# Optimization experiments

Measured on AMD Instinct MI355X. Metric: run time of the kernel, lower is better.

## Reference

```python
import jax, jax.numpy as jnp
import numpy as np

B, T, H, Q = 64, 2048, 512, 512


def setup_inputs() -> dict:
    key = jax.random.key(0)
    k1, k2, k3, k4, k5 = jax.random.split(key, 5)
    query = jax.random.normal(k1, (B, Q), dtype=jnp.float32)
    encoder_outputs = jax.random.normal(k2, (B, T, H), dtype=jnp.float32)
    # nn.Linear(hidden_size, query_size): weight [Q, H], bias [Q]
    W = jax.random.normal(k3, (Q, H), dtype=jnp.float32) * (1.0 / np.sqrt(H))
    b = jax.random.normal(k4, (Q,), dtype=jnp.float32) * 0.01
    tgt_index = jax.random.randint(k5, (B,), 0, T, dtype=jnp.int64)
    return {"query": query, "encoder_outputs": encoder_outputs, "W": W, "b": b,
            "tgt_index": tgt_index}


def reference(query, encoder_outputs, W, b, tgt_index):
    # method == 'general': energy[b,i] = (W @ enc[b,i] + bias) . query[b]
    proj = jnp.einsum('bth,qh->btq', encoder_outputs, W) + b       # [B,T,Q]
    energies = jnp.einsum('btq,bq->bt', proj, query)               # [B,T]
    # ragged mask: position i valid iff i <= tgt_index[b] (this_len = tgt_index+1)
    mask = jnp.arange(T)[None, :] <= tgt_index[:, None]            # [B,T]
    logits = jnp.where(mask, energies, -jnp.inf)
    attn = jax.nn.softmax(logits, axis=-1)                         # [B,T]
    context = jnp.einsum('bt,bth->bh', attn, encoder_outputs)      # [B,H]
    return context
```

## Files before the change

kernel.cpp:

```cpp
#include <hip/hip_runtime.h>
#include <hip/hip_bf16.h>
#include <math.h>


#define B 64
#define T 2048
#define H 512
#define Q 512
#define TT 128
#define NCH (T / TT)

__global__ void k_proj(const float* __restrict__ query,
                       const float* __restrict__ W,
                       const float* __restrict__ bias,
                       float* __restrict__ v,
                       float* __restrict__ c) {
    int b = blockIdx.y;
    int tid = threadIdx.x;
    int h = blockIdx.x * 128 + tid;

    __shared__ float sq[Q];
    for (int i = tid; i < Q; i += 128) sq[i] = query[(size_t)b * Q + i];
    __syncthreads();

    float acc = 0.0f;
#pragma unroll 8
    for (int q = 0; q < Q; ++q) acc += sq[q] * W[(size_t)q * H + h];
    v[(size_t)b * H + h] = acc;

    if (blockIdx.x == 0) {
        float pb = 0.0f;
        for (int i = tid; i < Q; i += 128) pb += sq[i] * bias[i];
        for (int off = 32; off; off >>= 1) pb += __shfl_xor(pb, off, 64);
        __shared__ float sred[2];
        if ((tid & 63) == 0) sred[tid >> 6] = pb;
        __syncthreads();
        if (tid == 0) c[b] = sred[0] + sred[1];
    }
}

__global__ __launch_bounds__(256) void k_attn(const float* __restrict__ enc,
                                              const float* __restrict__ v,
                                              const float* __restrict__ c,
                                              const int* __restrict__ tgt,
                                              float* __restrict__ pm,
                                              float* __restrict__ pl,
                                              float* __restrict__ pctx) {
    int b = blockIdx.y;
    int len = tgt[b] + 1;
    int t0 = blockIdx.x * TT;
    if (t0 >= len) return;
    int n = min(TT, len - t0);

    int tid = threadIdx.x;
    int wave = tid >> 6;
    int lane = tid & 63;

    const float4* v4 = (const float4*)(v + (size_t)b * H);
    float4 w0 = v4[lane];
    float4 w1 = v4[lane + 64];
    float cb = c[b];

    float m = -INFINITY, l = 0.0f;
    float4 a0 = {0.f,0.f,0.f,0.f}, a1 = {0.f,0.f,0.f,0.f};
    const float* encb = enc + ((size_t)b * T + t0) * H;

    for (int t = wave * 4; t < n; t += 16) {
        const float4* r0 = (const float4*)(encb + (size_t)(t + 0) * H);
        const float4* r1 = (const float4*)(encb + (size_t)(t + 1) * H);
        const float4* r2 = (const float4*)(encb + (size_t)(t + 2) * H);
        const float4* r3 = (const float4*)(encb + (size_t)(t + 3) * H);
        float4 x00 = r0[lane], x01 = r0[lane + 64];
        float4 x10 = r1[lane], x11 = r1[lane + 64];
        float4 x20 = r2[lane], x21 = r2[lane + 64];
        float4 x30 = r3[lane], x31 = r3[lane + 64];

        float e0 = x00.x*w0.x + x00.y*w0.y + x00.z*w0.z + x00.w*w0.w
                 + x01.x*w1.x + x01.y*w1.y + x01.z*w1.z + x01.w*w1.w;
        float e1 = x10.x*w0.x + x10.y*w0.y + x10.z*w0.z + x10.w*w0.w
                 + x11.x*w1.x + x11.y*w1.y + x11.z*w1.z + x11.w*w1.w;
        float e2 = x20.x*w0.x + x20.y*w0.y + x20.z*w0.z + x20.w*w0.w
                 + x21.x*w1.x + x21.y*w1.y + x21.z*w1.z + x21.w*w1.w;
        float e3 = x30.x*w0.x + x30.y*w0.y + x30.z*w0.z + x30.w*w0.w
                 + x31.x*w1.x + x31.y*w1.y + x31.z*w1.z + x31.w*w1.w;

        for (int off = 32; off; off >>= 1) {
            e0 += __shfl_xor(e0, off, 64);
            e1 += __shfl_xor(e1, off, 64);
            e2 += __shfl_xor(e2, off, 64);
            e3 += __shfl_xor(e3, off, 64);
        }
        e0 += cb;
        e1 = (t + 1 < n) ? e1 + cb : -INFINITY;
        e2 = (t + 2 < n) ? e2 + cb : -INFINITY;
        e3 = (t + 3 < n) ? e3 + cb : -INFINITY;

        float mn = fmaxf(fmaxf(fmaxf(e0, e1), fmaxf(e2, e3)), m);
        float alpha = __expf(m - mn);
        float p0 = __expf(e0 - mn);
        float p1 = __expf(e1 - mn);
        float p2 = __expf(e2 - mn);
        float p3 = __expf(e3 - mn);
        l = l * alpha + (p0 + p1) + (p2 + p3);
        a0.x = a0.x*alpha + p0*x00.x + p1*x10.x + p2*x20.x + p3*x30.x;
        a0.y = a0.y*alpha + p0*x00.y + p1*x10.y + p2*x20.y + p3*x30.y;
        a0.z = a0.z*alpha + p0*x00.z + p1*x10.z + p2*x20.z + p3*x30.z;
        a0.w = a0.w*alpha + p0*x00.w + p1*x10.w + p2*x20.w + p3*x30.w;
        a1.x = a1.x*alpha + p0*x01.x + p1*x11.x + p2*x21.x + p3*x31.x;
        a1.y = a1.y*alpha + p0*x01.y + p1*x11.y + p2*x21.y + p3*x31.y;
        a1.z = a1.z*alpha + p0*x01.z + p1*x11.z + p2*x21.z + p3*x31.z;
        a1.w = a1.w*alpha + p0*x01.w + p1*x11.w + p2*x21.w + p3*x31.w;
        m = mn;
    }

    __shared__ float sm4[4], sl4[4];
    __shared__ float sctx[4 * H];
    float4* sc = (float4*)(sctx + wave * H);
    sc[lane]      = a0;
    sc[lane + 64] = a1;
    if (lane == 0) { sm4[wave] = m; sl4[wave] = l; }
    __syncthreads();

    float M = fmaxf(fmaxf(sm4[0], sm4[1]), fmaxf(sm4[2], sm4[3]));
    float L = 0.0f, acc0 = 0.0f, acc1 = 0.0f;
#pragma unroll
    for (int j = 0; j < 4; ++j) {
        float mj = sm4[j];
        float wj = (mj == -INFINITY) ? 0.0f : __expf(mj - M);
        L += sl4[j] * wj;
        acc0 += wj * sctx[j * H + 2 * tid];
        acc1 += wj * sctx[j * H + 2 * tid + 1];
    }
    int pidx = b * NCH + blockIdx.x;
    if (tid == 0) { pm[pidx] = M; pl[pidx] = L; }
    float2* dst = (float2*)(pctx + (size_t)pidx * H);
    dst[tid] = make_float2(acc0, acc1);
}

__global__ void k_combine(const float* __restrict__ pm,
                          const float* __restrict__ pl,
                          const float* __restrict__ pctx,
                          const int* __restrict__ tgt,
                          float* __restrict__ out) {
    int b = blockIdx.x;
    int tid = threadIdx.x;
    int len = tgt[b] + 1;
    int nch = (len + TT - 1) / TT;

    __shared__ float spm[NCH], spl[NCH];
    if (tid < nch) {
        spm[tid] = pm[b * NCH + tid];
        spl[tid] = pl[b * NCH + tid];
    }
    __syncthreads();

    float M = -INFINITY;
    for (int j = 0; j < nch; ++j) M = fmaxf(M, spm[j]);
    float L = 0.0f;
    for (int j = 0; j < nch; ++j) L += spl[j] * __expf(spm[j] - M);
    float invL = 1.0f / L;

    float acc0 = 0.0f, acc1 = 0.0f;
    for (int j = 0; j < nch; ++j) {
        float wj = __expf(spm[j] - M) * invL;
        float2 x = ((const float2*)(pctx + (size_t)(b * NCH + j) * H))[tid];
        acc0 += wj * x.x;
        acc1 += wj * x.y;
    }
    out[(size_t)b * H + 2 * tid]     = acc0;
    out[(size_t)b * H + 2 * tid + 1] = acc1;
}

extern "C" void kernel_launch(void* const* d_in, const int* in_sizes, int n_in,
                              void* d_out, int out_size, void* d_ws, size_t ws_size,
                              hipStream_t stream) {
    const float* query = (const float*)d_in[0];
    const float* enc   = (const float*)d_in[1];
    const float* W     = (const float*)d_in[2];
    const float* bias  = (const float*)d_in[3];
    const int*   tgt   = (const int*)d_in[4];
    float* out = (float*)d_out;

    char* ws = (char*)d_ws;
    float* v    = (float*)ws;  ws += (size_t)B * H * sizeof(float);
    float* c    = (float*)ws;  ws += 256;
    float* pm   = (float*)ws;  ws += (size_t)B * NCH * sizeof(float);
    float* pl   = (float*)ws;  ws += (size_t)B * NCH * sizeof(float);
    float* pctx = (float*)ws;

    k_proj<<<dim3(H / 128, B), dim3(128), 0, stream>>>(query, W, bias, v, c);
    k_attn<<<dim3(NCH, B), dim3(256), 0, stream>>>(enc, v, c, tgt, pm, pl, pctx);
    k_combine<<<dim3(B), dim3(256), 0, stream>>>(pm, pl, pctx, tgt, out);
}
```

Measured before the change: 378.5 us.

## Fuse combine into attention via last-block atomic counter and vectorize projection kernel

```diff
diff --git a/kernel.cpp b/kernel.cpp
--- a/kernel.cpp
+++ b/kernel.cpp
@@ -1,5 +1,4 @@
 #include <hip/hip_runtime.h>
-#include <hip/hip_bf16.h>
 #include <math.h>
 
 
@@ -10,32 +9,56 @@
 #define TT 128
 #define NCH (T / TT)
 
-__global__ void k_proj(const float* __restrict__ query,
-                       const float* __restrict__ W,
-                       const float* __restrict__ bias,
-                       float* __restrict__ v,
-                       float* __restrict__ c) {
+__global__ __launch_bounds__(256) void k_proj(const float* __restrict__ query,
+                                              const float* __restrict__ W,
+                                              const float* __restrict__ bias,
+                                              float* __restrict__ v,
+                                              float* __restrict__ c,
+                                              int* __restrict__ cnt) {
     int b = blockIdx.y;
     int tid = threadIdx.x;
-    int h = blockIdx.x * 128 + tid;
+    int lane = tid & 63;
+    int qq = tid >> 6;
+    int h4 = blockIdx.x * 256 + lane * 4;
 
     __shared__ float sq[Q];
-    for (int i = tid; i < Q; i += 128) sq[i] = query[(size_t)b * Q + i];
-    __syncthreads();
-
-    float acc = 0.0f;
+    ((float2*)sq)[tid] = ((const float2*)(query + (size_t)b * Q))[tid];
+    __syncthreads();
+
+    float4 acc = {0.f, 0.f, 0.f, 0.f};
+    const float* Wp = W + (size_t)(qq * 128) * H + h4;
 #pragma unroll 8
-    for (int q = 0; q < Q; ++q) acc += sq[q] * W[(size_t)q * H + h];
-    v[(size_t)b * H + h] = acc;
+    for (int q = 0; q < 128; ++q) {
+        float s = sq[qq * 128 + q];
+        const float4 w = *(const float4*)(Wp + (size_t)q * H);
+        acc.x += s * w.x; acc.y += s * w.y;
+        acc.z += s * w.z; acc.w += s * w.w;
+    }
+
+    __shared__ float4 sp[4][64];
+    sp[qq][lane] = acc;
+    __syncthreads();
+    if (qq == 0) {
+        float4 r0 = sp[0][lane], r1 = sp[1][lane];
+        float4 r2 = sp[2][lane], r3 = sp[3][lane];
+        float4 r;
+        r.x = (r0.x + r1.x) + (r2.x + r3.x);
+        r.y = (r0.y + r1.y) + (r2.y + r3.y);
+        r.z = (r0.z + r1.z) + (r2.z + r3.z);
+        r.w = (r0.w + r1.w) + (r2.w + r3.w);
+        ((float4*)(v + (size_t)b * H))[blockIdx.x * 64 + lane] = r;
+    }
 
     if (blockIdx.x == 0) {
-        float pb = 0.0f;
-        for (int i = tid; i < Q; i += 128) pb += sq[i] * bias[i];
+        float pb = sq[tid] * bias[tid] + sq[tid + 256] * bias[tid + 256];
         for (int off = 32; off; off >>= 1) pb += __shfl_xor(pb, off, 64);
-        __shared__ float sred[2];
-        if ((tid & 63) == 0) sred[tid >> 6] = pb;
+        __shared__ float sred[4];
+        if (lane == 0) sred[qq] = pb;
         __syncthreads();
-        if (tid == 0) c[b] = sred[0] + sred[1];
+        if (tid == 0) {
+            c[b] = (sred[0] + sred[1]) + (sred[2] + sred[3]);
+            cnt[b] = 0;
+        }
     }
 }
 
@@ -45,12 +68,15 @@
                                               const int* __restrict__ tgt,
                                               float* __restrict__ pm,
                                               float* __restrict__ pl,
-                                              float* __restrict__ pctx) {
+                                              float* __restrict__ pctx,
+                                              int* __restrict__ cnt,
+                                              float* __restrict__ out) {
     int b = blockIdx.y;
     int len = tgt[b] + 1;
     int t0 = blockIdx.x * TT;
     if (t0 >= len) return;
     int n = min(TT, len - t0);
+    int nch = (len + TT - 1) / TT;
 
     int tid = threadIdx.x;
     int wave = tid >> 6;
@@ -135,17 +161,16 @@
     if (tid == 0) { pm[pidx] = M; pl[pidx] = L; }
     float2* dst = (float2*)(pctx + (size_t)pidx * H);
     dst[tid] = make_float2(acc0, acc1);
-}
-
-__global__ void k_combine(const float* __restrict__ pm,
-                          const float* __restrict__ pl,
-                          const float* __restrict__ pctx,
-                          const int* __restrict__ tgt,
-                          float* __restrict__ out) {
-    int b = blockIdx.x;
-    int tid = threadIdx.x;
-    int len = tgt[b] + 1;
-    int nch = (len + TT - 1) / TT;
+
+    __syncthreads();
+    __shared__ int slast;
+    if (tid == 0) {
+        __threadfence();
+        slast = (atomicAdd(&cnt[b], 1) == nch - 1);
+    }
+    __syncthreads();
+    if (!slast) return;
+    __threadfence();
 
     __shared__ float spm[NCH], spl[NCH];
     if (tid < nch) {
@@ -154,21 +179,21 @@
     }
     __syncthreads();
 
-    float M = -INFINITY;
-    for (int j = 0; j < nch; ++j) M = fmaxf(M, spm[j]);
-    float L = 0.0f;
-    for (int j = 0; j < nch; ++j) L += spl[j] * __expf(spm[j] - M);
-    float invL = 1.0f / L;
-
-    float acc0 = 0.0f, acc1 = 0.0f;
+    float M2 = -INFINITY;
+    for (int j = 0; j < nch; ++j) M2 = fmaxf(M2, spm[j]);
+    float L2 = 0.0f;
+    for (int j = 0; j < nch; ++j) L2 += spl[j] * __expf(spm[j] - M2);
+    float invL = 1.0f / L2;
+
+    float o0 = 0.0f, o1 = 0.0f;
     for (int j = 0; j < nch; ++j) {
-        float wj = __expf(spm[j] - M) * invL;
+        float wj = __expf(spm[j] - M2) * invL;
         float2 x = ((const float2*)(pctx + (size_t)(b * NCH + j) * H))[tid];
-        acc0 += wj * x.x;
-        acc1 += wj * x.y;
-    }
-    out[(size_t)b * H + 2 * tid]     = acc0;
-    out[(size_t)b * H + 2 * tid + 1] = acc1;
+        o0 += wj * x.x;
+        o1 += wj * x.y;
+    }
+    out[(size_t)b * H + 2 * tid]     = o0;
+    out[(size_t)b * H + 2 * tid + 1] = o1;
 }
 
 extern "C" void kernel_launch(void* const* d_in, const int* in_sizes, int n_in,
@@ -186,9 +211,10 @@
     float* c    = (float*)ws;  ws += 256;
     float* pm   = (float*)ws;  ws += (size_t)B * NCH * sizeof(float);
     float* pl   = (float*)ws;  ws += (size_t)B * NCH * sizeof(float);
-    float* pctx = (float*)ws;
-
-    k_proj<<<dim3(H / 128, B), dim3(128), 0, stream>>>(query, W, bias, v, c);
-    k_attn<<<dim3(NCH, B), dim3(256), 0, stream>>>(enc, v, c, tgt, pm, pl, pctx);
-    k_combine<<<dim3(B), dim3(256), 0, stream>>>(pm, pl, pctx, tgt, out);
+    float* pctx = (float*)ws;  ws += (size_t)B * NCH * H * sizeof(float);
+    int*   cnt  = (int*)ws;
+
+    k_proj<<<dim3(2, B), dim3(256), 0, stream>>>(query, W, bias, v, c, cnt);
+    k_attn<<<dim3(NCH, B), dim3(256), 0, stream>>>(enc, v, c, tgt,
+                                                   pm, pl, pctx, cnt, out);
 }
```

Result: slower. 470.1 us (+24.2%).

## Shrink attention chunk size and vectorize projection kernel with split-Q reduction

Applied to the files above, without the earlier changes.

```diff
diff --git a/kernel.cpp b/kernel.cpp
--- a/kernel.cpp
+++ b/kernel.cpp
@@ -1,5 +1,4 @@
 #include <hip/hip_runtime.h>
-#include <hip/hip_bf16.h>
 #include <math.h>
 
 
@@ -7,35 +6,55 @@
 #define T 2048
 #define H 512
 #define Q 512
-#define TT 128
+#define TT 32
 #define NCH (T / TT)
 
-__global__ void k_proj(const float* __restrict__ query,
-                       const float* __restrict__ W,
-                       const float* __restrict__ bias,
-                       float* __restrict__ v,
-                       float* __restrict__ c) {
+__global__ __launch_bounds__(256) void k_proj(const float* __restrict__ query,
+                                              const float* __restrict__ W,
+                                              const float* __restrict__ bias,
+                                              float* __restrict__ v,
+                                              float* __restrict__ c) {
     int b = blockIdx.y;
     int tid = threadIdx.x;
-    int h = blockIdx.x * 128 + tid;
+    int lane = tid & 63;
+    int qq = tid >> 6;
+    int h4 = blockIdx.x * 256 + lane * 4;
 
     __shared__ float sq[Q];
-    for (int i = tid; i < Q; i += 128) sq[i] = query[(size_t)b * Q + i];
-    __syncthreads();
-
-    float acc = 0.0f;
+    ((float2*)sq)[tid] = ((const float2*)(query + (size_t)b * Q))[tid];
+    __syncthreads();
+
+    float4 acc = {0.f, 0.f, 0.f, 0.f};
+    const float* Wp = W + (size_t)(qq * 128) * H + h4;
 #pragma unroll 8
-    for (int q = 0; q < Q; ++q) acc += sq[q] * W[(size_t)q * H + h];
-    v[(size_t)b * H + h] = acc;
+    for (int q = 0; q < 128; ++q) {
+        float s = sq[qq * 128 + q];
+        const float4 w = *(const float4*)(Wp + (size_t)q * H);
+        acc.x += s * w.x; acc.y += s * w.y;
+        acc.z += s * w.z; acc.w += s * w.w;
+    }
+
+    __shared__ float4 sp[4][64];
+    sp[qq][lane] = acc;
+    __syncthreads();
+    if (qq == 0) {
+        float4 r0 = sp[0][lane], r1 = sp[1][lane];
+        float4 r2 = sp[2][lane], r3 = sp[3][lane];
+        float4 r;
+        r.x = (r0.x + r1.x) + (r2.x + r3.x);
+        r.y = (r0.y + r1.y) + (r2.y + r3.y);
+        r.z = (r0.z + r1.z) + (r2.z + r3.z);
+        r.w = (r0.w + r1.w) + (r2.w + r3.w);
+        ((float4*)(v + (size_t)b * H))[blockIdx.x * 64 + lane] = r;
+    }
 
     if (blockIdx.x == 0) {
-        float pb = 0.0f;
-        for (int i = tid; i < Q; i += 128) pb += sq[i] * bias[i];
+        float pb = sq[tid] * bias[tid] + sq[tid + 256] * bias[tid + 256];
         for (int off = 32; off; off >>= 1) pb += __shfl_xor(pb, off, 64);
-        __shared__ float sred[2];
-        if ((tid & 63) == 0) sred[tid >> 6] = pb;
+        __shared__ float sred[4];
+        if (lane == 0) sred[qq] = pb;
         __syncthreads();
-        if (tid == 0) c[b] = sred[0] + sred[1];
+        if (tid == 0) c[b] = (sred[0] + sred[1]) + (sred[2] + sred[3]);
     }
 }
 
@@ -161,6 +180,7 @@
     float invL = 1.0f / L;
 
     float acc0 = 0.0f, acc1 = 0.0f;
+#pragma unroll 4
     for (int j = 0; j < nch; ++j) {
         float wj = __expf(spm[j] - M) * invL;
         float2 x = ((const float2*)(pctx + (size_t)(b * NCH + j) * H))[tid];
@@ -188,7 +208,7 @@
     float* pl   = (float*)ws;  ws += (size_t)B * NCH * sizeof(float);
     float* pctx = (float*)ws;
 
-    k_proj<<<dim3(H / 128, B), dim3(128), 0, stream>>>(query, W, bias, v, c);
+    k_proj<<<dim3(2, B), dim3(256), 0, stream>>>(query, W, bias, v, c);
     k_attn<<<dim3(NCH, B), dim3(256), 0, stream>>>(enc, v, c, tgt, pm, pl, pctx);
     k_combine<<<dim3(B), dim3(256), 0, stream>>>(pm, pl, pctx, tgt, out);
 }
```

Measured after the change: 354.4 us. -6.4%, faster.
